# Kernel tuning notes

Hardware: AMD Instinct MI355X
Metric: run time of the kernel (lower is better)

## Reference

```python
import jax, jax.numpy as jnp
import numpy as np

D_MODEL = 1024
D_STATE = 16
D_CONV = 4
EXPAND = 2
D_INNER = D_MODEL * EXPAND
B = 1
L = 2048


def setup_inputs() -> dict:
    key = jax.random.key(0)
    ks = jax.random.split(key, 8)
    s = lambda k, shape, scale: jax.random.normal(k, shape, dtype=jnp.float32) * scale
    return {
        "x": jax.random.normal(ks[0], (B, L, D_MODEL), dtype=jnp.float32),
        "in_proj_w": s(ks[1], (D_INNER * 2, D_MODEL), D_MODEL ** -0.5),
        "conv_w": s(ks[2], (D_INNER, 1, D_CONV), D_CONV ** -0.5),  # depthwise [O, I/g=1, K]
        "conv_b": jnp.zeros((D_INNER,), jnp.float32),
        "x_proj_w": s(ks[3], (2 * D_STATE + 1, D_INNER), D_INNER ** -0.5),
        "dt_proj_w": s(ks[4], (D_INNER, 1), 1.0),
        "dt_proj_b": jnp.zeros((D_INNER,), jnp.float32),
        "A_log": jnp.log(jnp.broadcast_to(jnp.arange(1, D_STATE + 1, dtype=jnp.float32), (D_INNER, D_STATE))),
        "D": jnp.ones((D_INNER,), jnp.float32),
        "out_proj_w": s(ks[5], (D_MODEL, D_INNER), D_INNER ** -0.5),
    }


def reference(x, in_proj_w, conv_w, conv_b, x_proj_w, dt_proj_w, dt_proj_b, A_log, D, out_proj_w):
    Bb = x.shape[0]
    # in_proj -> split into ssm branch and gate z
    xz = x @ in_proj_w.T                      # [B, L, 2*Di]
    x_ssm, z = jnp.split(xz, 2, axis=-1)
    # causal depthwise conv1d (torch pads K-1 both sides then slices [:L] == left-pad K-1)
    xt = jnp.swapaxes(x_ssm, 1, 2)            # [B, Di, L]
    xc = jax.lax.conv_general_dilated(
        xt, conv_w, window_strides=(1,), padding=[(D_CONV - 1, 0)],
        feature_group_count=D_INNER, dimension_numbers=("NCH", "OIH", "NCH"))
    xc = xc + conv_b[None, :, None]
    xc = jax.nn.silu(jnp.swapaxes(xc, 1, 2))  # [B, L, Di]
    # selective SSM
    A = -jnp.exp(A_log)                        # [Di, N]
    xp = xc @ x_proj_w.T                       # [B, L, 1+2N]
    dt_r = xp[..., :1]
    Bv = xp[..., 1:1 + D_STATE]                # [B, L, N]
    Cv = xp[..., 1 + D_STATE:]                 # [B, L, N]
    dt = jax.nn.softplus(dt_r @ dt_proj_w.T + dt_proj_b)   # [B, L, Di]
    dA = jnp.exp(dt[..., None] * A)                          # [B, L, Di, N]
    dBx = dt[..., None] * Bv[:, :, None, :] * xc[..., None]  # [B, L, Di, N]

    def step(h, inps):
        dA_t, dBx_t, C_t = inps
        h = dA_t * h + dBx_t                   # [B, Di, N]
        y = jnp.einsum("bdn,bn->bd", h, C_t)
        return h, y

    h0 = jnp.zeros((Bb, D_INNER, D_STATE), x.dtype)
    _, ys = jax.lax.scan(step, h0, (jnp.swapaxes(dA, 0, 1), jnp.swapaxes(dBx, 0, 1), jnp.swapaxes(Cv, 0, 1)))
    y = jnp.swapaxes(ys, 0, 1) + xc * D        # [B, L, Di]
    return (y * jax.nn.silu(z)) @ out_proj_w.T
```

## Files before the change

kernel.cpp:

```cpp
#include <hip/hip_runtime.h>
#include <math.h>

#define L_SEQ   2048
#define DM      1024
#define DI      2048
#define NST     16
#define LC      32
#define NCHUNK  64
#define XP_LD   36
#define KSPLIT  8

typedef short s16x8 __attribute__((ext_vector_type(8)));
typedef float f32x4 __attribute__((ext_vector_type(4)));

__device__ __forceinline__ float silu_f(float x) {
  return x / (1.0f + __expf(-x));
}
__device__ __forceinline__ float softplus_f(float x) {
  return x > 20.0f ? x : log1pf(__expf(x));
}
__device__ __forceinline__ ushort f2bf(float f) {
  unsigned int u = __float_as_uint(f);
  unsigned int r = (u + 0x7fffu + ((u >> 16) & 1u)) >> 16;
  return (ushort)r;
}
__device__ __forceinline__ void gload_lds16(const void* g, void* lds) {
  __builtin_amdgcn_global_load_lds(
      (const __attribute__((address_space(1))) unsigned int*)g,
      (__attribute__((address_space(3))) unsigned int*)lds,
      16, 0, 0);
}

__global__ __launch_bounds__(256) void cvt_bf16_k(
    const float* __restrict__ in, ushort* __restrict__ out, int n4) {
  int i = blockIdx.x * 256 + threadIdx.x;
  if (i >= n4) return;
  float4 v = ((const float4*)in)[i];
  ushort4 o;
  o.x = f2bf(v.x); o.y = f2bf(v.y); o.z = f2bf(v.z); o.w = f2bf(v.w);
  ((ushort4*)out)[i] = o;
}

template <int MFRAG>
__global__ __launch_bounds__(256) void gemm_mfma_bf16(
    const ushort* __restrict__ A, const ushort* __restrict__ B,
    float* __restrict__ C, int K, int ldc) {
  constexpr int BM = MFRAG * 32;
  __shared__ ushort As[BM * 32];
  __shared__ ushort Bs[128 * 32];
  const int tid  = threadIdx.x;
  const int lane = tid & 63;
  const int wv   = tid >> 6;
  const int wr   = wv >> 1;
  const int wc   = wv & 1;
  const int m0 = blockIdx.y * BM;
  const int n0 = blockIdx.x * 128;

  f32x4 acc[MFRAG][4] = {};

  const int kc = (tid & 3) * 8;

  for (int k0 = 0; k0 < K; k0 += 32) {
    __syncthreads();
#pragma unroll
    for (int q = 0; q < BM / 64; ++q) {
      int id = q * 256 + tid;
      int m  = id >> 2;
      gload_lds16(A + (size_t)(m0 + m) * K + k0 + kc, (char*)As + id * 16);
    }
#pragma unroll
    for (int q = 0; q < 2; ++q) {
      int id = q * 256 + tid;
      int n  = id >> 2;
      gload_lds16(B + (size_t)(n0 + n) * K + k0 + kc, (char*)Bs + id * 16);
    }
    __syncthreads();

    s16x8 af[MFRAG], bfr[4];
#pragma unroll
    for (int m = 0; m < MFRAG; ++m)
      af[m] = *(const s16x8*)&As[(wr * MFRAG * 16 + m * 16 + (lane & 15)) * 32 + (lane >> 4) * 8];
#pragma unroll
    for (int n = 0; n < 4; ++n)
      bfr[n] = *(const s16x8*)&Bs[(wc * 64 + n * 16 + (lane & 15)) * 32 + (lane >> 4) * 8];
#pragma unroll
    for (int m = 0; m < MFRAG; ++m)
#pragma unroll
      for (int n = 0; n < 4; ++n)
        acc[m][n] = __builtin_amdgcn_mfma_f32_16x16x32_bf16(af[m], bfr[n], acc[m][n], 0, 0, 0);
  }
  const int cr = (lane >> 4) * 4;
  const int cc = lane & 15;
#pragma unroll
  for (int m = 0; m < MFRAG; ++m) {
    int gr0 = m0 + wr * MFRAG * 16 + m * 16 + cr;
#pragma unroll
    for (int n = 0; n < 4; ++n) {
      int gc = n0 + wc * 64 + n * 16 + cc;
#pragma unroll
      for (int r = 0; r < 4; ++r)
        C[(size_t)(gr0 + r) * ldc + gc] = acc[m][n][r];
    }
  }
}

__global__ __launch_bounds__(256) void conv_silu_k(
    const float* __restrict__ xz, const float* __restrict__ cw,
    const float* __restrict__ cb, float* __restrict__ xc) {
  const int d = blockIdx.x * 256 + threadIdx.x;
  const int l = blockIdx.y;
  const float w0 = cw[d*4+0], w1 = cw[d*4+1], w2 = cw[d*4+2], w3 = cw[d*4+3];
  float acc = cb[d];
  if (l >= 3) acc = fmaf(w0, xz[(size_t)(l-3)*4096 + d], acc);
  if (l >= 2) acc = fmaf(w1, xz[(size_t)(l-2)*4096 + d], acc);
  if (l >= 1) acc = fmaf(w2, xz[(size_t)(l-1)*4096 + d], acc);
  acc = fmaf(w3, xz[(size_t)l*4096 + d], acc);
  xc[(size_t)l*DI + d] = silu_f(acc);
}

__global__ __launch_bounds__(256) void gemm_xp_k(
    const float* __restrict__ xc, const float* __restrict__ Wxp,
    float* __restrict__ xp_part) {
  const int L0   = blockIdx.x * 64;
  const int ks   = blockIdx.y;
  const int wv   = threadIdx.x >> 6;
  const int lane = threadIdx.x & 63;
  __shared__ float xcs[64][65];
  __shared__ float Ws[36][64];
  float acc[9] = {};
  const int kbeg = ks * (DI / KSPLIT);
  const int kend = kbeg + DI / KSPLIT;
  for (int k0 = kbeg; k0 < kend; k0 += 64) {
    {
      int r = threadIdx.x >> 2;
      int cbase = (threadIdx.x & 3) * 16;
#pragma unroll
      for (int q = 0; q < 4; ++q) {
        float4 v = *(const float4*)&xc[(size_t)(L0 + r) * DI + k0 + cbase + q*4];
        xcs[r][cbase + q*4 + 0] = v.x; xcs[r][cbase + q*4 + 1] = v.y;
        xcs[r][cbase + q*4 + 2] = v.z; xcs[r][cbase + q*4 + 3] = v.w;
      }
    }
    for (int idx = threadIdx.x; idx < 36 * 16; idx += 256) {
      int j = idx >> 4; int cc = (idx & 15) << 2;
      float4 v = make_float4(0.f, 0.f, 0.f, 0.f);
      if (j < 33) v = *(const float4*)&Wxp[(size_t)j * DI + k0 + cc];
      *(float4*)&Ws[j][cc] = v;
    }
    __syncthreads();
#pragma unroll 4
    for (int kk = 0; kk < 64; kk += 4) {
      float4 wr[9];
#pragma unroll
      for (int jj = 0; jj < 9; ++jj) wr[jj] = *(const float4*)&Ws[wv*9 + jj][kk];
      float a0 = xcs[lane][kk+0], a1 = xcs[lane][kk+1];
      float a2 = xcs[lane][kk+2], a3 = xcs[lane][kk+3];
#pragma unroll
      for (int jj = 0; jj < 9; ++jj) {
        acc[jj] = fmaf(a0, wr[jj].x, acc[jj]);
        acc[jj] = fmaf(a1, wr[jj].y, acc[jj]);
        acc[jj] = fmaf(a2, wr[jj].z, acc[jj]);
        acc[jj] = fmaf(a3, wr[jj].w, acc[jj]);
      }
    }
    __syncthreads();
  }
  const int l = L0 + lane;
#pragma unroll
  for (int jj = 0; jj < 9; ++jj) {
    int j = wv * 9 + jj;
    if (j < 33)
      xp_part[(size_t)ks * L_SEQ * XP_LD + (size_t)l * XP_LD + j] = acc[jj];
  }
}

__global__ __launch_bounds__(256) void reduce_xp_k(
    const float* __restrict__ part, float* __restrict__ xp) {
  int i = blockIdx.x * 256 + threadIdx.x;
  float s = 0.f;
#pragma unroll
  for (int ks = 0; ks < KSPLIT; ++ks)
    s += part[(size_t)ks * L_SEQ * XP_LD + i];
  xp[i] = s;
}

__global__ __launch_bounds__(256) void scan_partial_k(
    const float* __restrict__ xc, const float* __restrict__ xp,
    const float* __restrict__ dtw, const float* __restrict__ dtb,
    const float* __restrict__ A_log,
    float* __restrict__ P, float* __restrict__ Q) {
  const int tid = threadIdx.x;
  const int d   = blockIdx.x * 128 + (tid >> 1);
  const int nb  = (tid & 1) * 8;
  const int c   = blockIdx.y;
  const int l0  = c * LC;
  __shared__ float xps[LC][33];
  for (int idx = tid; idx < LC * 33; idx += 256) {
    int rr = idx / 33, cc = idx - rr * 33;
    xps[rr][cc] = xp[(size_t)(l0 + rr) * XP_LD + cc];
  }
  float Ad[8];
#pragma unroll
  for (int j4 = 0; j4 < 8; j4 += 4) {
    float4 v = *(const float4*)&A_log[(size_t)d * NST + nb + j4];
    Ad[j4+0] = -__expf(v.x); Ad[j4+1] = -__expf(v.y);
    Ad[j4+2] = -__expf(v.z); Ad[j4+3] = -__expf(v.w);
  }
  const float w = dtw[d], b = dtb[d];
  float h[8], p[8];
#pragma unroll
  for (int n = 0; n < 8; ++n) { h[n] = 0.f; p[n] = 1.f; }
  __syncthreads();
  const float* xcp = xc + (size_t)l0 * DI + d;
  for (int t = 0; t < LC; ++t) {
    float xcv = xcp[(size_t)t * DI];
    float dt  = softplus_f(fmaf(xps[t][0], w, b));
    float dtx = dt * xcv;
#pragma unroll
    for (int n = 0; n < 8; ++n) {
      float da = __expf(dt * Ad[n]);
      h[n] = fmaf(da, h[n], dtx * xps[t][1 + nb + n]);
      p[n] *= da;
    }
  }
  size_t base = ((size_t)c * DI + d) * NST + nb;
  *(float4*)&P[base]     = make_float4(p[0], p[1], p[2], p[3]);
  *(float4*)&P[base + 4] = make_float4(p[4], p[5], p[6], p[7]);
  *(float4*)&Q[base]     = make_float4(h[0], h[1], h[2], h[3]);
  *(float4*)&Q[base + 4] = make_float4(h[4], h[5], h[6], h[7]);
}

__global__ __launch_bounds__(256) void scan_prefix_k(
    const float* __restrict__ P, float* __restrict__ QHs) {
  const int g = blockIdx.x * 256 + threadIdx.x;
  const int d = g >> 2;
  const int q = (g & 3) << 2;
  float4 h = make_float4(0.f, 0.f, 0.f, 0.f);
#pragma unroll 8
  for (int c = 0; c < NCHUNK; ++c) {
    size_t base = ((size_t)c * DI + d) * NST + q;
    float4 pv = *(const float4*)&P[base];
    float4 qv = *(const float4*)&QHs[base];
    *(float4*)&QHs[base] = h;
    h.x = fmaf(pv.x, h.x, qv.x);
    h.y = fmaf(pv.y, h.y, qv.y);
    h.z = fmaf(pv.z, h.z, qv.z);
    h.w = fmaf(pv.w, h.w, qv.w);
  }
}

__global__ __launch_bounds__(256) void scan_final_k(
    const float* __restrict__ xc, const float* __restrict__ xp,
    const float* __restrict__ dtw, const float* __restrict__ dtb,
    const float* __restrict__ A_log, const float* __restrict__ Dp,
    const float* __restrict__ Hs, const float* __restrict__ xz,
    ushort* __restrict__ ys) {
  const int tid  = threadIdx.x;
  const int d    = blockIdx.x * 128 + (tid >> 1);
  const int half = tid & 1;
  const int nb   = half * 8;
  const int c    = blockIdx.y;
  const int l0   = c * LC;
  __shared__ float xps[LC][33];
  for (int idx = tid; idx < LC * 33; idx += 256) {
    int rr = idx / 33, cc = idx - rr * 33;
    xps[rr][cc] = xp[(size_t)(l0 + rr) * XP_LD + cc];
  }
  float Ad[8];
#pragma unroll
  for (int j4 = 0; j4 < 8; j4 += 4) {
    float4 v = *(const float4*)&A_log[(size_t)d * NST + nb + j4];
    Ad[j4+0] = -__expf(v.x); Ad[j4+1] = -__expf(v.y);
    Ad[j4+2] = -__expf(v.z); Ad[j4+3] = -__expf(v.w);
  }
  const float w = dtw[d], b = dtb[d], Dd = Dp[d];
  float h[8];
  size_t hb = ((size_t)c * DI + d) * NST + nb;
  *(float4*)&h[0] = *(const float4*)&Hs[hb];
  *(float4*)&h[4] = *(const float4*)&Hs[hb + 4];
  __syncthreads();
  for (int t = 0; t < LC; ++t) {
    const int l = l0 + t;
    float xcv = xc[(size_t)l * DI + d];
    float dt  = softplus_f(fmaf(xps[t][0], w, b));
    float dtx = dt * xcv;
    float y = 0.f;
#pragma unroll
    for (int n = 0; n < 8; ++n) {
      float da = __expf(dt * Ad[n]);
      h[n] = fmaf(da, h[n], dtx * xps[t][1 + nb + n]);
      y = fmaf(h[n], xps[t][17 + nb + n], y);
    }
    y += __shfl_xor(y, 1);
    if (half == 0) {
      y = fmaf(xcv, Dd, y);
      float zv = xz[(size_t)l * 4096 + 2048 + d];
      ys[(size_t)l * DI + d] = f2bf(y * silu_f(zv));
    }
  }
}

extern "C" void kernel_launch(void* const* d_in, const int* in_sizes, int n_in,
                              void* d_out, int out_size, void* d_ws, size_t ws_size,
                              hipStream_t stream) {
  const float* x    = (const float*)d_in[0];
  const float* W1   = (const float*)d_in[1];
  const float* cw   = (const float*)d_in[2];
  const float* cb   = (const float*)d_in[3];
  const float* Wxp  = (const float*)d_in[4];
  const float* dtw  = (const float*)d_in[5];
  const float* dtb  = (const float*)d_in[6];
  const float* Alog = (const float*)d_in[7];
  const float* Dp   = (const float*)d_in[8];
  const float* Wout = (const float*)d_in[9];
  float* out = (float*)d_out;

  char* w = (char*)d_ws;
  float*  xz      = (float*)w;
  float*  xc      = (float*)(w + 33554432);
  float*  xp      = (float*)(w + 50331648);
  ushort* x_bf    = (ushort*)(w + 50626560);
  ushort* W1_bf   = (ushort*)(w + 54820864);
  float*  xp_part = (float*)(w + 50626560);
  float*  P       = (float*)(w + 50626560);
  float*  QHs     = (float*)(w + 59015168);
  ushort* Wout_bf = (ushort*)(w + 67403776);
  ushort* ys_bf   = (ushort*)(w + 71598080);

  cvt_bf16_k<<<2048, 256, 0, stream>>>(x,    x_bf,    2048*1024/4);
  cvt_bf16_k<<<4096, 256, 0, stream>>>(W1,   W1_bf,   4096*1024/4);
  cvt_bf16_k<<<2048, 256, 0, stream>>>(Wout, Wout_bf, 1024*2048/4);
  gemm_mfma_bf16<4><<<dim3(4096/128, 2048/128), 256, 0, stream>>>(x_bf, W1_bf, xz, DM, 4096);
  conv_silu_k<<<dim3(DI/256, L_SEQ), 256, 0, stream>>>(xz, cw, cb, xc);
  gemm_xp_k<<<dim3(L_SEQ/64, KSPLIT), 256, 0, stream>>>(xc, Wxp, xp_part);
  reduce_xp_k<<<L_SEQ*XP_LD/256, 256, 0, stream>>>(xp_part, xp);
  scan_partial_k<<<dim3(DI/128, NCHUNK), 256, 0, stream>>>(xc, xp, dtw, dtb, Alog, P, QHs);
  scan_prefix_k<<<DI*NST/4/256, 256, 0, stream>>>(P, QHs);
  scan_final_k<<<dim3(DI/128, NCHUNK), 256, 0, stream>>>(xc, xp, dtw, dtb, Alog, Dp, QHs, xz, ys_bf);
  gemm_mfma_bf16<2><<<dim3(1024/128, 2048/64), 256, 0, stream>>>(ys_bf, Wout_bf, out, DI, 1024);
}
```

Baseline: 304.2 us.

## Transpose xc for per-thread contiguous scan loads and prefetch z into registers

Adds a tiled transpose kernel that stores the conv output as [D_INNER, L], so each scan thread loads its 32-step chunk of xc with float4 loads before the loop. The scan kernels also preload the gate z values, move dt to the end of a padded shared row so B and C can be read as vec4 LDS loads, and fully unroll the time loop. The aim is to take latency-bound per-step global loads off the sequential recurrence. In exchange it adds an extra 16MB read and write pass for the transpose, raises register pressure, and reshuffles workspace aliasing.

Result: slower. 429.7 us (+41.2%).

```diff
diff --git a/kernel.cpp b/kernel.cpp
--- a/kernel.cpp
+++ b/kernel.cpp
@@ -116,6 +116,32 @@
   if (l >= 1) acc = fmaf(w2, xz[(size_t)(l-1)*4096 + d], acc);
   acc = fmaf(w3, xz[(size_t)l*4096 + d], acc);
   xc[(size_t)l*DI + d] = silu_f(acc);
+}
+
+__global__ __launch_bounds__(256) void transpose_k(
+    const float* __restrict__ in, float* __restrict__ out) {
+  __shared__ float tile[64][65];
+  const int d0 = blockIdx.x * 64, l0 = blockIdx.y * 64;
+  const int r  = threadIdx.x >> 4;
+  const int c4 = (threadIdx.x & 15) * 4;
+#pragma unroll
+  for (int p = 0; p < 4; ++p) {
+    float4 v = *(const float4*)&in[(size_t)(l0 + r + p*16) * DI + d0 + c4];
+    tile[r + p*16][c4+0] = v.x; tile[r + p*16][c4+1] = v.y;
+    tile[r + p*16][c4+2] = v.z; tile[r + p*16][c4+3] = v.w;
+  }
+  __syncthreads();
+  const int dd = threadIdx.x >> 4;
+  const int l4 = (threadIdx.x & 15) * 4;
+#pragma unroll
+  for (int p = 0; p < 4; ++p) {
+    float4 v;
+    v.x = tile[l4+0][dd + p*16];
+    v.y = tile[l4+1][dd + p*16];
+    v.z = tile[l4+2][dd + p*16];
+    v.w = tile[l4+3][dd + p*16];
+    *(float4*)&out[(size_t)(d0 + dd + p*16) * L_SEQ + l0 + l4] = v;
+  }
 }
 
 __global__ __launch_bounds__(256) void gemm_xp_k(
@@ -184,8 +210,17 @@
   xp[i] = s;
 }
 
+__device__ __forceinline__ void stage_xps(
+    float (*xps)[36], const float* __restrict__ xp, int l0, int tid) {
+  for (int idx = tid; idx < LC * 33; idx += 256) {
+    int rr = idx / 33, j = idx - rr * 33;
+    int col = (j == 0) ? 32 : j - 1;
+    xps[rr][col] = xp[(size_t)(l0 + rr) * XP_LD + j];
+  }
+}
+
 __global__ __launch_bounds__(256) void scan_partial_k(
-    const float* __restrict__ xc, const float* __restrict__ xp,
+    const float* __restrict__ xcT, const float* __restrict__ xp,
     const float* __restrict__ dtw, const float* __restrict__ dtb,
     const float* __restrict__ A_log,
     float* __restrict__ P, float* __restrict__ Q) {
@@ -194,10 +229,14 @@
   const int nb  = (tid & 1) * 8;
   const int c   = blockIdx.y;
   const int l0  = c * LC;
-  __shared__ float xps[LC][33];
-  for (int idx = tid; idx < LC * 33; idx += 256) {
-    int rr = idx / 33, cc = idx - rr * 33;
-    xps[rr][cc] = xp[(size_t)(l0 + rr) * XP_LD + cc];
+  __shared__ float xps[LC][36];
+  stage_xps(xps, xp, l0, tid);
+
+  float xcf[LC];
+  {
+    const float4* src = (const float4*)(xcT + (size_t)d * L_SEQ + l0);
+#pragma unroll
+    for (int q = 0; q < LC/4; ++q) *(float4*)&xcf[q*4] = src[q];
   }
   float Ad[8];
 #pragma unroll
@@ -211,15 +250,18 @@
 #pragma unroll
   for (int n = 0; n < 8; ++n) { h[n] = 0.f; p[n] = 1.f; }
   __syncthreads();
-  const float* xcp = xc + (size_t)l0 * DI + d;
+#pragma unroll
   for (int t = 0; t < LC; ++t) {
-    float xcv = xcp[(size_t)t * DI];
-    float dt  = softplus_f(fmaf(xps[t][0], w, b));
-    float dtx = dt * xcv;
+    float dt  = softplus_f(fmaf(xps[t][32], w, b));
+    float dtx = dt * xcf[t];
+    f32x4 B0 = *(const f32x4*)&xps[t][nb];
+    f32x4 B1 = *(const f32x4*)&xps[t][nb + 4];
+    float Bv[8];
+    *(f32x4*)&Bv[0] = B0; *(f32x4*)&Bv[4] = B1;
 #pragma unroll
     for (int n = 0; n < 8; ++n) {
       float da = __expf(dt * Ad[n]);
-      h[n] = fmaf(da, h[n], dtx * xps[t][1 + nb + n]);
+      h[n] = fmaf(da, h[n], dtx * Bv[n]);
       p[n] *= da;
     }
   }
@@ -250,7 +292,7 @@
 }
 
 __global__ __launch_bounds__(256) void scan_final_k(
-    const float* __restrict__ xc, const float* __restrict__ xp,
+    const float* __restrict__ xcT, const float* __restrict__ xp,
     const float* __restrict__ dtw, const float* __restrict__ dtb,
     const float* __restrict__ A_log, const float* __restrict__ Dp,
     const float* __restrict__ Hs, const float* __restrict__ xz,
@@ -261,11 +303,20 @@
   const int nb   = half * 8;
   const int c    = blockIdx.y;
   const int l0   = c * LC;
-  __shared__ float xps[LC][33];
-  for (int idx = tid; idx < LC * 33; idx += 256) {
-    int rr = idx / 33, cc = idx - rr * 33;
-    xps[rr][cc] = xp[(size_t)(l0 + rr) * XP_LD + cc];
-  }
+  __shared__ float xps[LC][36];
+  stage_xps(xps, xp, l0, tid);
+
+  float xcf[LC];
+  {
+    const float4* src = (const float4*)(xcT + (size_t)d * L_SEQ + l0);
+#pragma unroll
+    for (int q = 0; q < LC/4; ++q) *(float4*)&xcf[q*4] = src[q];
+  }
+  float zbuf[LC];
+#pragma unroll
+  for (int t = 0; t < LC; ++t)
+    zbuf[t] = xz[(size_t)(l0 + t) * 4096 + 2048 + d];
+
   float Ad[8];
 #pragma unroll
   for (int j4 = 0; j4 < 8; j4 += 4) {
@@ -279,23 +330,29 @@
   *(float4*)&h[0] = *(const float4*)&Hs[hb];
   *(float4*)&h[4] = *(const float4*)&Hs[hb + 4];
   __syncthreads();
+#pragma unroll
   for (int t = 0; t < LC; ++t) {
     const int l = l0 + t;
-    float xcv = xc[(size_t)l * DI + d];
-    float dt  = softplus_f(fmaf(xps[t][0], w, b));
-    float dtx = dt * xcv;
+    float dt  = softplus_f(fmaf(xps[t][32], w, b));
+    float dtx = dt * xcf[t];
+    f32x4 B0 = *(const f32x4*)&xps[t][nb];
+    f32x4 B1 = *(const f32x4*)&xps[t][nb + 4];
+    f32x4 C0 = *(const f32x4*)&xps[t][16 + nb];
+    f32x4 C1 = *(const f32x4*)&xps[t][20 + nb];
+    float Bv[8], Cv[8];
+    *(f32x4*)&Bv[0] = B0; *(f32x4*)&Bv[4] = B1;
+    *(f32x4*)&Cv[0] = C0; *(f32x4*)&Cv[4] = C1;
     float y = 0.f;
 #pragma unroll
     for (int n = 0; n < 8; ++n) {
       float da = __expf(dt * Ad[n]);
-      h[n] = fmaf(da, h[n], dtx * xps[t][1 + nb + n]);
-      y = fmaf(h[n], xps[t][17 + nb + n], y);
+      h[n] = fmaf(da, h[n], dtx * Bv[n]);
+      y = fmaf(h[n], Cv[n], y);
     }
     y += __shfl_xor(y, 1);
     if (half == 0) {
-      y = fmaf(xcv, Dd, y);
-      float zv = xz[(size_t)l * 4096 + 2048 + d];
-      ys[(size_t)l * DI + d] = f2bf(y * silu_f(zv));
+      y = fmaf(xcf[t], Dd, y);
+      ys[(size_t)l * DI + d] = f2bf(y * silu_f(zbuf[t]));
     }
   }
 }
@@ -317,25 +374,27 @@
 
   char* w = (char*)d_ws;
   float*  xz      = (float*)w;
-  float*  xc      = (float*)(w + 33554432);
-  float*  xp      = (float*)(w + 50331648);
-  ushort* x_bf    = (ushort*)(w + 50626560);
-  ushort* W1_bf   = (ushort*)(w + 54820864);
-  float*  xp_part = (float*)(w + 50626560);
-  float*  P       = (float*)(w + 50626560);
-  float*  QHs     = (float*)(w + 59015168);
+  float*  xcT     = (float*)(w + 33554432);
+  float*  xc_rm   = (float*)(w + 50331648);
+  ushort* x_bf    = (ushort*)(w + 50331648);
+  ushort* W1_bf   = (ushort*)(w + 54525952);
+  float*  P       = (float*)(w + 50331648);
+  float*  QHs     = (float*)(w + 58720256);
+  float*  xp      = (float*)(w + 67108864);
   ushort* Wout_bf = (ushort*)(w + 67403776);
   ushort* ys_bf   = (ushort*)(w + 71598080);
+  float*  xp_part = (float*)(w + 71598080);
 
   cvt_bf16_k<<<2048, 256, 0, stream>>>(x,    x_bf,    2048*1024/4);
   cvt_bf16_k<<<4096, 256, 0, stream>>>(W1,   W1_bf,   4096*1024/4);
   cvt_bf16_k<<<2048, 256, 0, stream>>>(Wout, Wout_bf, 1024*2048/4);
   gemm_mfma_bf16<4><<<dim3(4096/128, 2048/128), 256, 0, stream>>>(x_bf, W1_bf, xz, DM, 4096);
-  conv_silu_k<<<dim3(DI/256, L_SEQ), 256, 0, stream>>>(xz, cw, cb, xc);
-  gemm_xp_k<<<dim3(L_SEQ/64, KSPLIT), 256, 0, stream>>>(xc, Wxp, xp_part);
+  conv_silu_k<<<dim3(DI/256, L_SEQ), 256, 0, stream>>>(xz, cw, cb, xc_rm);
+  transpose_k<<<dim3(DI/64, L_SEQ/64), 256, 0, stream>>>(xc_rm, xcT);
+  gemm_xp_k<<<dim3(L_SEQ/64, KSPLIT), 256, 0, stream>>>(xc_rm, Wxp, xp_part);
   reduce_xp_k<<<L_SEQ*XP_LD/256, 256, 0, stream>>>(xp_part, xp);
-  scan_partial_k<<<dim3(DI/128, NCHUNK), 256, 0, stream>>>(xc, xp, dtw, dtb, Alog, P, QHs);
+  scan_partial_k<<<dim3(DI/128, NCHUNK), 256, 0, stream>>>(xcT, xp, dtw, dtb, Alog, P, QHs);
   scan_prefix_k<<<DI*NST/4/256, 256, 0, stream>>>(P, QHs);
-  scan_final_k<<<dim3(DI/128, NCHUNK), 256, 0, stream>>>(xc, xp, dtw, dtb, Alog, Dp, QHs, xz, ys_bf);
+  scan_final_k<<<dim3(DI/128, NCHUNK), 256, 0, stream>>>(xcT, xp, dtw, dtb, Alog, Dp, QHs, xz, ys_bf);
   gemm_mfma_bf16<2><<<dim3(1024/128, 2048/64), 256, 0, stream>>>(ys_bf, Wout_bf, out, DI, 1024);
 }
```
